# Kernel tuning notes

Hardware: AMD Instinct MI355X
Metric: run time of the kernel (lower is better)

Reference implementation:

```python
import jax, jax.numpy as jnp
import numpy as np

B, N, M, HA, HB, H = 16, 256, 12, 64, 64, 4
DIN = 2 * HA + HB
DOUT = 4 * H * HA


def _bn(x, g, b, eps=1e-5):
    # BatchNorm1d forward with batch statistics (training-mode math), x: [R, C]
    m = jnp.mean(x, axis=0)
    v = jnp.var(x, axis=0)
    return (x - m) * jax.lax.rsqrt(v + eps) * g + b


def setup_inputs() -> dict:
    key = jax.random.key(0)
    ks = jax.random.split(key, 6)
    atom_emb = jax.random.normal(ks[0], (B, N, HA), jnp.float32)
    nbr_emb = jax.random.normal(ks[1], (B, N, M, HB), jnp.float32)
    nbr_adj_list = jax.random.randint(ks[2], (B, N, M), 0, N)
    atom_mask = jnp.ones((B, N, 1), jnp.float32)
    W_full = jax.random.normal(ks[3], (DIN, DOUT), jnp.float32) / np.sqrt(DIN)
    b_full = jnp.zeros((DOUT,), jnp.float32)
    W_final = jax.random.normal(ks[4], (H * HA, HA), jnp.float32) / np.sqrt(H * HA)
    b_final = jnp.zeros((HA,), jnp.float32)
    bn1_g = jnp.ones((HA,), jnp.float32)
    bn1_b = jnp.zeros((HA,), jnp.float32)
    bn2_g = jnp.ones((HA,), jnp.float32)
    bn2_b = jnp.zeros((HA,), jnp.float32)
    return dict(atom_emb=atom_emb, nbr_emb=nbr_emb, atom_mask=atom_mask,
                W_full=W_full, b_full=b_full, W_final=W_final, b_final=b_final,
                bn1_g=bn1_g, bn1_b=bn1_b, bn2_g=bn2_g, bn2_b=bn2_b,
                nbr_adj_list=nbr_adj_list)


def reference(atom_emb, nbr_emb, atom_mask, W_full, b_full, W_final, b_final,
              bn1_g, bn1_b, bn2_g, bn2_b, nbr_adj_list):
    # Gather neighbor atom embeddings: [B,N,M,HA]
    bidx = jnp.arange(B)[:, None, None]
    atom_nbr = atom_emb[bidx, nbr_adj_list]
    atom_nbr = atom_nbr * atom_mask[..., None]  # mask [B,N,1,1]

    mask3 = jnp.broadcast_to(atom_mask, (B, N, M))  # [B,N,M]

    # Concat self, neighbor, bond embeddings -> [B,N,M,2HA+HB]
    self_emb = jnp.broadcast_to(atom_emb[:, :, None, :], (B, N, M, HA))
    total = jnp.concatenate([self_emb, atom_nbr, nbr_emb], axis=-1)

    tg = total @ W_full + b_full  # [B,N,M,4*H*HA]
    gate, core, a1, a2 = jnp.split(tg, 4, axis=-1)
    core = core.reshape(B, N, M, H, HA)
    a1 = a1.reshape(B, N, M, H, HA)
    a2 = a2.reshape(B, N, M, H, HA)

    # Masked multi-head attention over the neighbor dim (M x M per atom)
    bias = (1.0 - mask3)[:, :, None, None, :] * -10000.0  # [B,N,1,1,M]
    scores = jnp.einsum('bnmhd,bnkhd->bnhmk', a1, a2) / np.sqrt(H) + bias
    probs = jax.nn.softmax(scores, axis=-1)  # dropout is identity in eval
    ctx = jnp.einsum('bnhmk,bnkhd->bnmhd', probs, core)  # [B,N,M,H,HA]

    core = jax.nn.relu(ctx)
    gate = jax.nn.sigmoid(gate.reshape(B, N, M, H, HA))
    summed = (gate * core).reshape(B, N, M, H * HA) @ W_final + b_final  # [B,N,M,HA]

    summed = _bn(summed.reshape(-1, HA), bn1_g, bn1_b).reshape(B, N, M, HA)
    summed = jax.nn.relu(summed)
    summed = jnp.sum(summed, axis=2)  # reduce over neighbors -> [B,N,HA]
    summed = _bn(summed.reshape(-1, HA), bn2_g, bn2_b).reshape(B, N, HA)
    return jax.nn.relu(atom_emb + summed)
```

## Files before the change

kernel.cpp:

```cpp
#include <hip/hip_runtime.h>
#include <hip/hip_bf16.h>

#define BB   16
#define NN   256
#define MM   12
#define HAc  64
#define Hh   4

#define PLD  264
#define TGLD 521

typedef __attribute__((ext_vector_type(8))) short bf16x8;
typedef __attribute__((ext_vector_type(4))) float f32x4;

__device__ __forceinline__ unsigned short f2bf(float x) {
    return __builtin_bit_cast(unsigned short, __float2bfloat16(x));
}
__device__ __forceinline__ float bf16f(unsigned short h) {
    unsigned u = ((unsigned)h) << 16;
    return __builtin_bit_cast(float, u);
}
__device__ __forceinline__ void split8(float4 a, float4 b, bf16x8& hi, bf16x8& lo) {
    float v[8] = {a.x, a.y, a.z, a.w, b.x, b.y, b.z, b.w};
    #pragma unroll
    for (int j = 0; j < 8; ++j) {
        unsigned short h = f2bf(v[j]);
        hi[j] = (short)h;
        lo[j] = (short)f2bf(v[j] - bf16f(h));
    }
}

__global__ __launch_bounds__(256) void k0a_pack(
    const float* __restrict__ W_full,
    const float* __restrict__ W_final,
    short* __restrict__ w12pk,
    short* __restrict__ w3pk,
    short* __restrict__ wfpk,
    float* __restrict__ zbase)
{
    const int t = threadIdx.x;
    if (blockIdx.x < 128) {
        const int gid  = blockIdx.x * 256 + t;
        const int lane = gid & 63;
        const int rest = gid >> 6;
        const int p  = rest & 1;
        const int ks = (rest >> 1) & 1;
        const int nt = rest >> 2;
        const int rbase = (nt >= 64 ? 64 : 0) + ks * 32 + (lane >> 4) * 8;
        const int n  = (nt & 63) * 16 + (lane & 15);
        bf16x8 o;
        #pragma unroll
        for (int j = 0; j < 8; ++j) {
            float v = W_full[(rbase + j) * 1024 + n];
            unsigned short h = f2bf(v);
            o[j] = p ? (short)f2bf(v - bf16f(h)) : (short)h;
        }
        *((bf16x8*)(w12pk + ((nt * 4 + ks * 2 + p) * 64 + lane) * 8)) = o;
    } else if (blockIdx.x < 192) {
        const int gid  = (blockIdx.x - 128) * 256 + t;
        const int lane = gid & 63;
        const int rest = gid >> 6;
        const int p  = rest & 1;
        const int ks = (rest >> 1) & 1;
        const int nt = rest >> 2;
        const int kb = ks * 32 + (lane >> 4) * 8;
        const int n  = nt * 16 + (lane & 15);
        bf16x8 o;
        #pragma unroll
        for (int j = 0; j < 8; ++j) {
            float v = W_full[(128 + kb + j) * 1024 + n];
            unsigned short h = f2bf(v);
            o[j] = p ? (short)f2bf(v - bf16f(h)) : (short)h;
        }
        *((bf16x8*)(w3pk + ((nt * 4 + ks * 2 + p) * 64 + lane) * 8)) = o;
    } else if (blockIdx.x < 208) {
        const int idx  = (blockIdx.x - 192) * 256 + t;
        const int lane = idx & 63;
        const int rest = idx >> 6;
        const int p  = rest & 1;
        const int ks = (rest >> 1) & 7;
        const int nt = rest >> 4;
        const int kb = ks * 32 + (lane >> 4) * 8;
        const int n  = nt * 16 + (lane & 15);
        bf16x8 o;
        #pragma unroll
        for (int j = 0; j < 8; ++j) {
            float v = W_final[(kb + j) * 64 + n];
            unsigned short h = f2bf(v);
            o[j] = p ? (short)f2bf(v - bf16f(h)) : (short)h;
        }
        *((bf16x8*)(wfpk + ((nt * 8 + ks) * 2 + p) * 512 + lane * 8)) = o;
    } else {
        const int gid = (blockIdx.x - 208) * 256 + t;
        if (gid < 8320) zbase[gid] = 0.f;
    }
}

__global__ __launch_bounds__(256) void k0b_p12(
    const float* __restrict__ atom_emb,
    const float* __restrict__ b_full,
    const short* __restrict__ w12pk,
    float* __restrict__ p1b,
    float* __restrict__ p2)
{
    const int r0   = blockIdx.x * 16;
    const int t    = threadIdx.x;
    const int w    = t >> 6;
    const int lane = t & 63;
    const int lr   = lane & 15;
    const int kg   = lane >> 4;

    bf16x8 aAh[2], aAl[2];
    #pragma unroll
    for (int ks = 0; ks < 2; ++ks) {
        const float4* ap = (const float4*)(atom_emb + (r0 + lr) * 64 + ks * 32 + kg * 8);
        split8(ap[0], ap[1], aAh[ks], aAl[ks]);
    }

    const bf16x8* W12P = (const bf16x8*)w12pk;
    #pragma unroll 4
    for (int i = 0; i < 16; ++i) {
        const int nt = w * 32 + blockIdx.y * 16 + i;
        bf16x8 Bh0 = W12P[(nt * 4 + 0) * 64 + lane];
        bf16x8 Bl0 = W12P[(nt * 4 + 1) * 64 + lane];
        bf16x8 Bh1 = W12P[(nt * 4 + 2) * 64 + lane];
        bf16x8 Bl1 = W12P[(nt * 4 + 3) * 64 + lane];
        const int n = (nt & 63) * 16 + lr;
        f32x4 acc;
        if (nt < 64) {
            float bv = b_full[n];
            acc[0] = bv; acc[1] = bv; acc[2] = bv; acc[3] = bv;
        } else {
            acc[0] = 0.f; acc[1] = 0.f; acc[2] = 0.f; acc[3] = 0.f;
        }
        acc = __builtin_amdgcn_mfma_f32_16x16x32_bf16(aAh[0], Bh0, acc, 0, 0, 0);
        acc = __builtin_amdgcn_mfma_f32_16x16x32_bf16(aAh[0], Bl0, acc, 0, 0, 0);
        acc = __builtin_amdgcn_mfma_f32_16x16x32_bf16(aAl[0], Bh0, acc, 0, 0, 0);
        acc = __builtin_amdgcn_mfma_f32_16x16x32_bf16(aAh[1], Bh1, acc, 0, 0, 0);
        acc = __builtin_amdgcn_mfma_f32_16x16x32_bf16(aAh[1], Bl1, acc, 0, 0, 0);
        acc = __builtin_amdgcn_mfma_f32_16x16x32_bf16(aAl[1], Bh1, acc, 0, 0, 0);
        float* dst = (nt < 64) ? p1b : p2;
        #pragma unroll
        for (int r = 0; r < 4; ++r)
            dst[(r0 + kg * 4 + r) * 1024 + n] = acc[r];
    }
}

__global__ __launch_bounds__(256) void k1_fused(
    const float* __restrict__ nbr_emb,
    const float* __restrict__ atom_mask,
    const float* __restrict__ p1b,
    const float* __restrict__ p2,
    const short* __restrict__ w3pk,
    const short* __restrict__ wfpk,
    const float* __restrict__ b_final,
    const int*   __restrict__ adj,
    float* __restrict__ pre,
    float* __restrict__ stats1b)
{
    __shared__ __align__(16) float tg[12][TGLD];
    __shared__ __align__(16) short a1hi[12 * PLD];
    __shared__ __align__(16) short a1lo[12 * PLD];
    __shared__ __align__(16) short a2hi[12 * PLD];
    __shared__ __align__(16) short a2lo[12 * PLD];
    __shared__ float scr[Hh][MM][MM];

    const int bn   = blockIdx.x;
    const int b    = bn >> 8;
    const int t    = threadIdx.x;
    const int w    = t >> 6;
    const int lane = t & 63;
    const int lr   = lane & 15;
    const int kg   = lane >> 4;
    const float mask = atom_mask[bn];

    bf16x8 nAhi[2], nAlo[2];
    #pragma unroll
    for (int ks = 0; ks < 2; ++ks) {
        float4 v0 = make_float4(0.f, 0.f, 0.f, 0.f), v1 = v0;
        if (lr < 12) {
            const float4* np = (const float4*)(nbr_emb + bn * 768 + lr * 64 + ks * 32 + kg * 8);
            v0 = np[0]; v1 = np[1];
        }
        split8(v0, v1, nAhi[ks], nAlo[ks]);
    }

    int nr[4];
    #pragma unroll
    for (int r = 0; r < 4; ++r) {
        int m = kg * 4 + r;
        nr[r] = (m < 12) ? (b * NN + adj[bn * MM + m]) : 0;
    }

    {
        const bf16x8* W3P = (const bf16x8*)w3pk;
        #pragma unroll 4
        for (int i = 0; i < 16; ++i) {
            const int nt = w * 16 + i;
            const int n  = nt * 16 + lr;
            bf16x8 B0h = W3P[(nt * 4 + 0) * 64 + lane];
            bf16x8 B0l = W3P[(nt * 4 + 1) * 64 + lane];
            bf16x8 B1h = W3P[(nt * 4 + 2) * 64 + lane];
            bf16x8 B1l = W3P[(nt * 4 + 3) * 64 + lane];
            const float p1v = p1b[bn * 1024 + n];
            f32x4 acc;
            #pragma unroll
            for (int r = 0; r < 4; ++r) {
                float pv = (kg * 4 + r < 12) ? p2[nr[r] * 1024 + n] : 0.f;
                acc[r] = p1v + mask * pv;
            }
            acc = __builtin_amdgcn_mfma_f32_16x16x32_bf16(nAhi[0], B0h, acc, 0, 0, 0);
            acc = __builtin_amdgcn_mfma_f32_16x16x32_bf16(nAhi[0], B0l, acc, 0, 0, 0);
            acc = __builtin_amdgcn_mfma_f32_16x16x32_bf16(nAlo[0], B0h, acc, 0, 0, 0);
            acc = __builtin_amdgcn_mfma_f32_16x16x32_bf16(nAhi[1], B1h, acc, 0, 0, 0);
            acc = __builtin_amdgcn_mfma_f32_16x16x32_bf16(nAhi[1], B1l, acc, 0, 0, 0);
            acc = __builtin_amdgcn_mfma_f32_16x16x32_bf16(nAlo[1], B1h, acc, 0, 0, 0);
            if (kg < 3) {
                if (w < 2) {
                    #pragma unroll
                    for (int r = 0; r < 4; ++r) tg[kg * 4 + r][n] = acc[r];
                } else {
                    const int cl = i * 16 + lr;
                    short* phi = (w == 2) ? a1hi : a2hi;
                    short* plo = (w == 2) ? a1lo : a2lo;
                    #pragma unroll
                    for (int r = 0; r < 4; ++r) {
                        const int row = kg * 4 + r;
                        unsigned short h = f2bf(acc[r]);
                        phi[row * PLD + cl] = (short)h;
                        plo[row * PLD + cl] = (short)f2bf(acc[r] - bf16f(h));
                    }
                }
            }
        }
    }
    __syncthreads();

    {
        const int h = w;
        f32x4 sc = {0.f, 0.f, 0.f, 0.f};
        #pragma unroll
        for (int ks = 0; ks < 2; ++ks) {
            bf16x8 x1h = {0,0,0,0,0,0,0,0}, x1l = x1h, x2h = x1h, x2l = x1h;
            if (lr < 12) {
                const int col = h * 64 + ks * 32 + kg * 8;
                x1h = *(const bf16x8*)&a1hi[lr * PLD + col];
                x1l = *(const bf16x8*)&a1lo[lr * PLD + col];
                x2h = *(const bf16x8*)&a2hi[lr * PLD + col];
                x2l = *(const bf16x8*)&a2lo[lr * PLD + col];
            }
            sc = __builtin_amdgcn_mfma_f32_16x16x32_bf16(x1h, x2h, sc, 0, 0, 0);
            sc = __builtin_amdgcn_mfma_f32_16x16x32_bf16(x1h, x2l, sc, 0, 0, 0);
            sc = __builtin_amdgcn_mfma_f32_16x16x32_bf16(x1l, x2h, sc, 0, 0, 0);
        }
        const float bias = (1.0f - mask) * (-10000.0f);
        if (kg < 3 && lr < 12) {
            #pragma unroll
            for (int r = 0; r < 4; ++r)
                scr[w][kg * 4 + r][lr] = 0.5f * sc[r] + bias;
        }
    }
    __syncthreads();

    if (t < Hh * MM) {
        float* row = &scr[0][0][0] + t * MM;
        float mx = row[0];
        #pragma unroll
        for (int k = 1; k < MM; ++k) mx = fmaxf(mx, row[k]);
        float e[MM];
        float sum = 0.f;
        #pragma unroll
        for (int k = 0; k < MM; ++k) { e[k] = __expf(row[k] - mx); sum += e[k]; }
        float inv = 1.0f / sum;
        #pragma unroll
        for (int k = 0; k < MM; ++k) row[k] = e[k] * inv;
    }
    __syncthreads();

    {
        const int c = t;
        const int h = c >> 6;
        float cv[MM];
        #pragma unroll
        for (int k = 0; k < MM; ++k) cv[k] = tg[k][256 + c];
        #pragma unroll
        for (int m = 0; m < MM; ++m) {
            float s = 0.f;
            #pragma unroll
            for (int k = 0; k < MM; ++k) s += scr[h][m][k] * cv[k];
            float gv = tg[m][c];
            float gt = 1.0f / (1.0f + __expf(-gv));
            float gc = gt * fmaxf(s, 0.f);
            unsigned short hh = f2bf(gc);
            a1hi[m * PLD + c] = (short)hh;
            a1lo[m * PLD + c] = (short)f2bf(gc - bf16f(hh));
        }
    }
    __syncthreads();

    {
        const bf16x8* WFP = (const bf16x8*)wfpk;
        f32x4 acc = {0.f, 0.f, 0.f, 0.f};
        #pragma unroll 2
        for (int ks = 0; ks < 8; ++ks) {
            bf16x8 Ah = {0,0,0,0,0,0,0,0}, Al = Ah;
            if (lr < 12) {
                const int col = ks * 32 + kg * 8;
                Ah = *(const bf16x8*)&a1hi[lr * PLD + col];
                Al = *(const bf16x8*)&a1lo[lr * PLD + col];
            }
            bf16x8 Bh = WFP[(w * 8 + ks) * 128 + lane];
            bf16x8 Bl = WFP[(w * 8 + ks) * 128 + 64 + lane];
            acc = __builtin_amdgcn_mfma_f32_16x16x32_bf16(Ah, Bh, acc, 0, 0, 0);
            acc = __builtin_amdgcn_mfma_f32_16x16x32_bf16(Ah, Bl, acc, 0, 0, 0);
            acc = __builtin_amdgcn_mfma_f32_16x16x32_bf16(Al, Bh, acc, 0, 0, 0);
        }
        const int n = w * 16 + lr;
        const float bf = b_final[n];
        float ssum = 0.f, ssq = 0.f;
        if (kg < 3) {
            #pragma unroll
            for (int r = 0; r < 4; ++r) {
                float v = acc[r] + bf;
                pre[(bn * MM + kg * 4 + r) * HAc + n] = v;
                ssum += v; ssq += v * v;
            }
        }
        ssum += __shfl_xor(ssum, 16); ssum += __shfl_xor(ssum, 32);
        ssq  += __shfl_xor(ssq, 16);  ssq  += __shfl_xor(ssq, 32);
        if (kg == 0) {
            const int bin = bn & 63;
            atomicAdd(&stats1b[bin * 128 + n], ssum);
            atomicAdd(&stats1b[bin * 128 + 64 + n], ssq);
        }
    }
}

__global__ __launch_bounds__(256) void k3_bn1_sum(const float* __restrict__ pre,
                                                  const float* __restrict__ stats1b,
                                                  const float* __restrict__ g1,
                                                  const float* __restrict__ b1,
                                                  float* __restrict__ tout,
                                                  float* __restrict__ stats2)
{
    const int t  = threadIdx.x;
    const int j  = t & 63;
    const int rg = t >> 6;

    __shared__ float sst[128];
    if (t < 128) {
        float s = 0.f;
        for (int bin = 0; bin < 64; ++bin) s += stats1b[bin * 128 + t];
        sst[t] = s;
    }
    __syncthreads();

    const float invR = 1.0f / 49152.0f;
    const float mean = sst[j] * invR;
    const float var  = sst[64 + j] * invR - mean * mean;
    const float rstd = rsqrtf(var + 1e-5f);
    const float ga = g1[j], be = b1[j];

    float s2 = 0.f, q2 = 0.f;
    for (int i = 0; i < 4; ++i) {
        const int bnrow = blockIdx.x * 16 + rg + i * 4;
        float s = 0.f;
        #pragma unroll
        for (int m = 0; m < MM; ++m) {
            float x = pre[(bnrow * MM + m) * HAc + j];
            float y = (x - mean) * rstd * ga + be;
            s += fmaxf(y, 0.f);
        }
        tout[bnrow * HAc + j] = s;
        s2 += s; q2 += s * s;
    }
    __shared__ float red[2][4][64];
    red[0][rg][j] = s2;
    red[1][rg][j] = q2;
    __syncthreads();
    if (t < 64) {
        float S = red[0][0][j] + red[0][1][j] + red[0][2][j] + red[0][3][j];
        float Q = red[1][0][j] + red[1][1][j] + red[1][2][j] + red[1][3][j];
        atomicAdd(&stats2[j], S);
        atomicAdd(&stats2[64 + j], Q);
    }
}

__global__ __launch_bounds__(256) void k4_bn2_out(const float* __restrict__ tin,
                                                  const float* __restrict__ stats2,
                                                  const float* __restrict__ g2,
                                                  const float* __restrict__ b2,
                                                  const float* __restrict__ atom_emb,
                                                  float* __restrict__ out)
{
    const int i4 = blockIdx.x * 256 + threadIdx.x;
    const int j0 = (i4 & 15) * 4;
    const float invR = 1.0f / 4096.0f;
    float4 tv = ((const float4*)tin)[i4];
    float4 ae = ((const float4*)atom_emb)[i4];
    float4 r;
    {
        float mean = stats2[j0] * invR;
        float var  = stats2[64 + j0] * invR - mean * mean;
        r.x = fmaxf(ae.x + (tv.x - mean) * rsqrtf(var + 1e-5f) * g2[j0] + b2[j0], 0.f);
    }
    {
        float mean = stats2[j0 + 1] * invR;
        float var  = stats2[64 + j0 + 1] * invR - mean * mean;
        r.y = fmaxf(ae.y + (tv.y - mean) * rsqrtf(var + 1e-5f) * g2[j0 + 1] + b2[j0 + 1], 0.f);
    }
    {
        float mean = stats2[j0 + 2] * invR;
        float var  = stats2[64 + j0 + 2] * invR - mean * mean;
        r.z = fmaxf(ae.z + (tv.z - mean) * rsqrtf(var + 1e-5f) * g2[j0 + 2] + b2[j0 + 2], 0.f);
    }
    {
        float mean = stats2[j0 + 3] * invR;
        float var  = stats2[64 + j0 + 3] * invR - mean * mean;
        r.w = fmaxf(ae.w + (tv.w - mean) * rsqrtf(var + 1e-5f) * g2[j0 + 3] + b2[j0 + 3], 0.f);
    }
    ((float4*)out)[i4] = r;
}

extern "C" void kernel_launch(void* const* d_in, const int* in_sizes, int n_in,
                              void* d_out, int out_size, void* d_ws, size_t ws_size,
                              hipStream_t stream)
{
    const float* atom_emb = (const float*)d_in[0];
    const float* nbr_emb  = (const float*)d_in[1];
    const float* atom_msk = (const float*)d_in[2];
    const float* W_full   = (const float*)d_in[3];
    const float* b_full   = (const float*)d_in[4];
    const float* W_final  = (const float*)d_in[5];
    const float* b_final  = (const float*)d_in[6];
    const float* bn1_g    = (const float*)d_in[7];
    const float* bn1_b    = (const float*)d_in[8];
    const float* bn2_g    = (const float*)d_in[9];
    const float* bn2_b    = (const float*)d_in[10];
    const int*   adj      = (const int*)d_in[11];
    float* out = (float*)d_out;

    float* ws      = (float*)d_ws;
    float* stats2  = ws;
    float* stats1b = ws + 128;
    float* p1b     = ws + 8320;
    float* p2      = p1b + 4194304;
    float* pre     = p2 + 4194304;
    short* w3pk    = (short*)(pre + 3145728);
    short* wfpk    = w3pk + 131072;
    short* w12pk   = wfpk + 32768;
    float* tout    = p1b;

    k0a_pack<<<241, 256, 0, stream>>>(W_full, W_final, w12pk, w3pk, wfpk, ws);
    k0b_p12<<<dim3(256, 2), 256, 0, stream>>>(atom_emb, b_full, w12pk, p1b, p2);
    k1_fused<<<BB * NN, 256, 0, stream>>>(nbr_emb, atom_msk, p1b, p2, w3pk, wfpk,
                                          b_final, adj, pre, stats1b);
    k3_bn1_sum<<<256, 256, 0, stream>>>(pre, stats1b, bn1_g, bn1_b, tout, stats2);
    k4_bn2_out<<<256, 256, 0, stream>>>(tout, stats2, bn2_g, bn2_b, atom_emb, out);
}
```

Measured before the change: 211.6 us.

## Merge weight-pack and P12 GEMM kernels; software-pipeline k1 gather loop

Merges the packing kernel and the atom projection GEMM into one launch. The GEMM blocks now read and split the fp32 W_full columns themselves instead of reading a prepacked w12 buffer, which removes a launch and the intermediate buffer at the cost of redundant per-block weight conversion. In the main fused kernel, the W3 tile, p1 and gathered p2 loads are double-buffered one iteration ahead of the MFMA chain. The p1/p2 addition moves after the MFMAs so the loads can overlap compute, at the cost of more live registers.

```diff
diff --git a/kernel.cpp b/kernel.cpp
--- a/kernel.cpp
+++ b/kernel.cpp
@@ -30,34 +30,69 @@
     }
 }
 
-__global__ __launch_bounds__(256) void k0a_pack(
+__global__ __launch_bounds__(256) void k0_prep(
+    const float* __restrict__ atom_emb,
     const float* __restrict__ W_full,
+    const float* __restrict__ b_full,
     const float* __restrict__ W_final,
-    short* __restrict__ w12pk,
+    float* __restrict__ p1b,
+    float* __restrict__ p2,
     short* __restrict__ w3pk,
     short* __restrict__ wfpk,
     float* __restrict__ zbase)
 {
     const int t = threadIdx.x;
-    if (blockIdx.x < 128) {
-        const int gid  = blockIdx.x * 256 + t;
-        const int lane = gid & 63;
-        const int rest = gid >> 6;
-        const int p  = rest & 1;
-        const int ks = (rest >> 1) & 1;
-        const int nt = rest >> 2;
-        const int rbase = (nt >= 64 ? 64 : 0) + ks * 32 + (lane >> 4) * 8;
-        const int n  = (nt & 63) * 16 + (lane & 15);
-        bf16x8 o;
-        #pragma unroll
-        for (int j = 0; j < 8; ++j) {
-            float v = W_full[(rbase + j) * 1024 + n];
-            unsigned short h = f2bf(v);
-            o[j] = p ? (short)f2bf(v - bf16f(h)) : (short)h;
-        }
-        *((bf16x8*)(w12pk + ((nt * 4 + ks * 2 + p) * 64 + lane) * 8)) = o;
-    } else if (blockIdx.x < 192) {
-        const int gid  = (blockIdx.x - 128) * 256 + t;
+    if (blockIdx.x < 512) {
+        const int q    = blockIdx.x;
+        const int r0   = (q >> 1) * 16;
+        const int half = q & 1;
+        const int w    = t >> 6;
+        const int lane = t & 63;
+        const int lr   = lane & 15;
+        const int kg   = lane >> 4;
+
+        bf16x8 aAh[2], aAl[2];
+        #pragma unroll
+        for (int ks = 0; ks < 2; ++ks) {
+            const float4* ap = (const float4*)(atom_emb + (r0 + lr) * 64 + ks * 32 + kg * 8);
+            split8(ap[0], ap[1], aAh[ks], aAl[ks]);
+        }
+
+        #pragma unroll 4
+        for (int i = 0; i < 16; ++i) {
+            const int nt   = w * 32 + half * 16 + i;
+            const int roff = (nt >= 64) ? 64 : 0;
+            const int ncol = (nt & 63) * 16 + lr;
+            bf16x8 Bh0, Bl0, Bh1, Bl1;
+            #pragma unroll
+            for (int j = 0; j < 8; ++j) {
+                float v0 = W_full[(roff + kg * 8 + j) * 1024 + ncol];
+                float v1 = W_full[(roff + 32 + kg * 8 + j) * 1024 + ncol];
+                unsigned short h0 = f2bf(v0);
+                Bh0[j] = (short)h0; Bl0[j] = (short)f2bf(v0 - bf16f(h0));
+                unsigned short h1 = f2bf(v1);
+                Bh1[j] = (short)h1; Bl1[j] = (short)f2bf(v1 - bf16f(h1));
+            }
+            f32x4 acc;
+            if (nt < 64) {
+                float bv = b_full[ncol];
+                acc[0] = bv; acc[1] = bv; acc[2] = bv; acc[3] = bv;
+            } else {
+                acc[0] = 0.f; acc[1] = 0.f; acc[2] = 0.f; acc[3] = 0.f;
+            }
+            acc = __builtin_amdgcn_mfma_f32_16x16x32_bf16(aAh[0], Bh0, acc, 0, 0, 0);
+            acc = __builtin_amdgcn_mfma_f32_16x16x32_bf16(aAh[0], Bl0, acc, 0, 0, 0);
+            acc = __builtin_amdgcn_mfma_f32_16x16x32_bf16(aAl[0], Bh0, acc, 0, 0, 0);
+            acc = __builtin_amdgcn_mfma_f32_16x16x32_bf16(aAh[1], Bh1, acc, 0, 0, 0);
+            acc = __builtin_amdgcn_mfma_f32_16x16x32_bf16(aAh[1], Bl1, acc, 0, 0, 0);
+            acc = __builtin_amdgcn_mfma_f32_16x16x32_bf16(aAl[1], Bh1, acc, 0, 0, 0);
+            float* dst = (nt < 64) ? p1b : p2;
+            #pragma unroll
+            for (int r = 0; r < 4; ++r)
+                dst[(r0 + kg * 4 + r) * 1024 + ncol] = acc[r];
+        }
+    } else if (blockIdx.x < 576) {
+        const int gid  = (blockIdx.x - 512) * 256 + t;
         const int lane = gid & 63;
         const int rest = gid >> 6;
         const int p  = rest & 1;
@@ -73,8 +108,8 @@
             o[j] = p ? (short)f2bf(v - bf16f(h)) : (short)h;
         }
         *((bf16x8*)(w3pk + ((nt * 4 + ks * 2 + p) * 64 + lane) * 8)) = o;
-    } else if (blockIdx.x < 208) {
-        const int idx  = (blockIdx.x - 192) * 256 + t;
+    } else if (blockIdx.x < 592) {
+        const int idx  = (blockIdx.x - 576) * 256 + t;
         const int lane = idx & 63;
         const int rest = idx >> 6;
         const int p  = rest & 1;
@@ -91,58 +126,8 @@
         }
         *((bf16x8*)(wfpk + ((nt * 8 + ks) * 2 + p) * 512 + lane * 8)) = o;
     } else {
-        const int gid = (blockIdx.x - 208) * 256 + t;
+        const int gid = (blockIdx.x - 592) * 256 + t;
         if (gid < 8320) zbase[gid] = 0.f;
-    }
-}
-
-__global__ __launch_bounds__(256) void k0b_p12(
-    const float* __restrict__ atom_emb,
-    const float* __restrict__ b_full,
-    const short* __restrict__ w12pk,
-    float* __restrict__ p1b,
-    float* __restrict__ p2)
-{
-    const int r0   = blockIdx.x * 16;
-    const int t    = threadIdx.x;
-    const int w    = t >> 6;
-    const int lane = t & 63;
-    const int lr   = lane & 15;
-    const int kg   = lane >> 4;
-
-    bf16x8 aAh[2], aAl[2];
-    #pragma unroll
-    for (int ks = 0; ks < 2; ++ks) {
-        const float4* ap = (const float4*)(atom_emb + (r0 + lr) * 64 + ks * 32 + kg * 8);
-        split8(ap[0], ap[1], aAh[ks], aAl[ks]);
-    }
-
-    const bf16x8* W12P = (const bf16x8*)w12pk;
-    #pragma unroll 4
-    for (int i = 0; i < 16; ++i) {
-        const int nt = w * 32 + blockIdx.y * 16 + i;
-        bf16x8 Bh0 = W12P[(nt * 4 + 0) * 64 + lane];
-        bf16x8 Bl0 = W12P[(nt * 4 + 1) * 64 + lane];
-        bf16x8 Bh1 = W12P[(nt * 4 + 2) * 64 + lane];
-        bf16x8 Bl1 = W12P[(nt * 4 + 3) * 64 + lane];
-        const int n = (nt & 63) * 16 + lr;
-        f32x4 acc;
-        if (nt < 64) {
-            float bv = b_full[n];
-            acc[0] = bv; acc[1] = bv; acc[2] = bv; acc[3] = bv;
-        } else {
-            acc[0] = 0.f; acc[1] = 0.f; acc[2] = 0.f; acc[3] = 0.f;
-        }
-        acc = __builtin_amdgcn_mfma_f32_16x16x32_bf16(aAh[0], Bh0, acc, 0, 0, 0);
-        acc = __builtin_amdgcn_mfma_f32_16x16x32_bf16(aAh[0], Bl0, acc, 0, 0, 0);
-        acc = __builtin_amdgcn_mfma_f32_16x16x32_bf16(aAl[0], Bh0, acc, 0, 0, 0);
-        acc = __builtin_amdgcn_mfma_f32_16x16x32_bf16(aAh[1], Bh1, acc, 0, 0, 0);
-        acc = __builtin_amdgcn_mfma_f32_16x16x32_bf16(aAh[1], Bl1, acc, 0, 0, 0);
-        acc = __builtin_amdgcn_mfma_f32_16x16x32_bf16(aAl[1], Bh1, acc, 0, 0, 0);
-        float* dst = (nt < 64) ? p1b : p2;
-        #pragma unroll
-        for (int r = 0; r < 4; ++r)
-            dst[(r0 + kg * 4 + r) * 1024 + n] = acc[r];
     }
 }
 
@@ -194,45 +179,64 @@
 
     {
         const bf16x8* W3P = (const bf16x8*)w3pk;
-        #pragma unroll 4
-        for (int i = 0; i < 16; ++i) {
-            const int nt = w * 16 + i;
-            const int n  = nt * 16 + lr;
-            bf16x8 B0h = W3P[(nt * 4 + 0) * 64 + lane];
-            bf16x8 B0l = W3P[(nt * 4 + 1) * 64 + lane];
-            bf16x8 B1h = W3P[(nt * 4 + 2) * 64 + lane];
-            bf16x8 B1l = W3P[(nt * 4 + 3) * 64 + lane];
-            const float p1v = p1b[bn * 1024 + n];
-            f32x4 acc;
-            #pragma unroll
-            for (int r = 0; r < 4; ++r) {
-                float pv = (kg * 4 + r < 12) ? p2[nr[r] * 1024 + n] : 0.f;
-                acc[r] = p1v + mask * pv;
-            }
-            acc = __builtin_amdgcn_mfma_f32_16x16x32_bf16(nAhi[0], B0h, acc, 0, 0, 0);
-            acc = __builtin_amdgcn_mfma_f32_16x16x32_bf16(nAhi[0], B0l, acc, 0, 0, 0);
-            acc = __builtin_amdgcn_mfma_f32_16x16x32_bf16(nAlo[0], B0h, acc, 0, 0, 0);
-            acc = __builtin_amdgcn_mfma_f32_16x16x32_bf16(nAhi[1], B1h, acc, 0, 0, 0);
-            acc = __builtin_amdgcn_mfma_f32_16x16x32_bf16(nAhi[1], B1l, acc, 0, 0, 0);
-            acc = __builtin_amdgcn_mfma_f32_16x16x32_bf16(nAlo[1], B1h, acc, 0, 0, 0);
-            if (kg < 3) {
-                if (w < 2) {
-                    #pragma unroll
-                    for (int r = 0; r < 4; ++r) tg[kg * 4 + r][n] = acc[r];
-                } else {
-                    const int cl = i * 16 + lr;
-                    short* phi = (w == 2) ? a1hi : a2hi;
-                    short* plo = (w == 2) ? a1lo : a2lo;
-                    #pragma unroll
-                    for (int r = 0; r < 4; ++r) {
-                        const int row = kg * 4 + r;
-                        unsigned short h = f2bf(acc[r]);
-                        phi[row * PLD + cl] = (short)h;
-                        plo[row * PLD + cl] = (short)f2bf(acc[r] - bf16f(h));
-                    }
-                }
-            }
-        }
+        const float* p1row = p1b + bn * 1024;
+
+        bf16x8 cB0h, cB0l, cB1h, cB1l; float cp1; f32x4 cp2;
+        bf16x8 xB0h, xB0l, xB1h, xB1l; float xp1; f32x4 xp2;
+
+#define PB_LOAD(IDX, B0h_, B0l_, B1h_, B1l_, P1_, P2_) do {                        \
+            const int nt_ = w * 16 + (IDX);                                         \
+            const int n_  = nt_ * 16 + lr;                                          \
+            B0h_ = W3P[(nt_ * 4 + 0) * 64 + lane];                                  \
+            B0l_ = W3P[(nt_ * 4 + 1) * 64 + lane];                                  \
+            B1h_ = W3P[(nt_ * 4 + 2) * 64 + lane];                                  \
+            B1l_ = W3P[(nt_ * 4 + 3) * 64 + lane];                                  \
+            P1_  = p1row[n_];                                                       \
+            _Pragma("unroll")                                                       \
+            for (int r_ = 0; r_ < 4; ++r_)                                          \
+                P2_[r_] = (kg * 4 + r_ < 12) ? p2[nr[r_] * 1024 + n_] : 0.f;        \
+        } while (0)
+
+#define PB_COMP(IDX, B0h_, B0l_, B1h_, B1l_, P1_, P2_) do {                        \
+            f32x4 acc = {0.f, 0.f, 0.f, 0.f};                                       \
+            acc = __builtin_amdgcn_mfma_f32_16x16x32_bf16(nAhi[0], B0h_, acc, 0, 0, 0); \
+            acc = __builtin_amdgcn_mfma_f32_16x16x32_bf16(nAhi[0], B0l_, acc, 0, 0, 0); \
+            acc = __builtin_amdgcn_mfma_f32_16x16x32_bf16(nAlo[0], B0h_, acc, 0, 0, 0); \
+            acc = __builtin_amdgcn_mfma_f32_16x16x32_bf16(nAhi[1], B1h_, acc, 0, 0, 0); \
+            acc = __builtin_amdgcn_mfma_f32_16x16x32_bf16(nAhi[1], B1l_, acc, 0, 0, 0); \
+            acc = __builtin_amdgcn_mfma_f32_16x16x32_bf16(nAlo[1], B1h_, acc, 0, 0, 0); \
+            const int n_ = (w * 16 + (IDX)) * 16 + lr;                              \
+            if (kg < 3) {                                                           \
+                if (w < 2) {                                                        \
+                    _Pragma("unroll")                                               \
+                    for (int r_ = 0; r_ < 4; ++r_)                                  \
+                        tg[kg * 4 + r_][n_] = acc[r_] + P1_ + mask * P2_[r_];       \
+                } else {                                                            \
+                    const int cl_ = (IDX) * 16 + lr;                                \
+                    short* phi_ = (w == 2) ? a1hi : a2hi;                           \
+                    short* plo_ = (w == 2) ? a1lo : a2lo;                           \
+                    _Pragma("unroll")                                               \
+                    for (int r_ = 0; r_ < 4; ++r_) {                                \
+                        float v_ = acc[r_] + P1_ + mask * P2_[r_];                  \
+                        unsigned short h_ = f2bf(v_);                               \
+                        phi_[(kg * 4 + r_) * PLD + cl_] = (short)h_;                \
+                        plo_[(kg * 4 + r_) * PLD + cl_] = (short)f2bf(v_ - bf16f(h_)); \
+                    }                                                               \
+                }                                                                   \
+            }                                                                       \
+        } while (0)
+
+        PB_LOAD(0, cB0h, cB0l, cB1h, cB1l, cp1, cp2);
+        for (int ii = 0; ii < 8; ++ii) {
+            const int i0 = 2 * ii, i1 = 2 * ii + 1;
+            PB_LOAD(i1, xB0h, xB0l, xB1h, xB1l, xp1, xp2);
+            PB_COMP(i0, cB0h, cB0l, cB1h, cB1l, cp1, cp2);
+            const int i2 = (i1 < 15) ? i1 + 1 : 15;
+            PB_LOAD(i2, cB0h, cB0l, cB1h, cB1l, cp1, cp2);
+            PB_COMP(i1, xB0h, xB0l, xB1h, xB1l, xp1, xp2);
+        }
+#undef PB_LOAD
+#undef PB_COMP
     }
     __syncthreads();
 
@@ -448,11 +452,10 @@
     float* pre     = p2 + 4194304;
     short* w3pk    = (short*)(pre + 3145728);
     short* wfpk    = w3pk + 131072;
-    short* w12pk   = wfpk + 32768;
     float* tout    = p1b;
 
-    k0a_pack<<<241, 256, 0, stream>>>(W_full, W_final, w12pk, w3pk, wfpk, ws);
-    k0b_p12<<<dim3(256, 2), 256, 0, stream>>>(atom_emb, b_full, w12pk, p1b, p2);
+    k0_prep<<<625, 256, 0, stream>>>(atom_emb, W_full, b_full, W_final,
+                                     p1b, p2, w3pk, wfpk, ws);
     k1_fused<<<BB * NN, 256, 0, stream>>>(nbr_emb, atom_msk, p1b, p2, w3pk, wfpk,
                                           b_final, adj, pre, stats1b);
     k3_bn1_sum<<<256, 256, 0, stream>>>(pre, stats1b, bn1_g, bn1_b, tout, stats2);
```

Measured after the change: 198.4 us. 6.2% less time.
